# Performance work log

Hardware: AMD Instinct MI355X
Metric: run time of the kernel (lower is better)

The kernel has to match this reference:

```python
import math
import jax, jax.numpy as jnp
import numpy as np

B, S, D, H = 2, 2048, 1024, 16
HD = D // H  # head_dim = 64


def setup_inputs() -> dict:
    key = jax.random.key(0)
    k1, k2, k3 = jax.random.split(key, 3)
    scale = 0.02
    return {
        "x": jax.random.normal(k1, (B, S, D), dtype=jnp.float32),
        "w_qkv": jax.random.normal(k2, (D, 3 * D), dtype=jnp.float32) * scale,
        "b_qkv": jnp.zeros((3 * D,), dtype=jnp.float32),
        "w_proj": jax.random.normal(k3, (D, D), dtype=jnp.float32) * scale,
        "b_proj": jnp.zeros((D,), dtype=jnp.float32),
    }


def reference(x, w_qkv, b_qkv, w_proj, b_proj):
    bsz, seq_len, d_model = x.shape
    # fused qkv projection: [B,S,3D] -> [3,B,H,S,HD]
    qkv = (x @ w_qkv + b_qkv).reshape(bsz, seq_len, 3, H, HD)
    qkv = jnp.transpose(qkv, (2, 0, 3, 1, 4))
    q, k, v = qkv[0], qkv[1], qkv[2]
    # scores [B,H,S,S]
    scores = jnp.einsum("bhqd,bhkd->bhqk", q, k) / math.sqrt(HD)
    causal = jnp.tril(jnp.ones((seq_len, seq_len), dtype=bool))
    scores = jnp.where(causal[None, None], scores, -jnp.inf)
    probs = jax.nn.softmax(scores, axis=-1)
    # dropout = 0.0 (eval mode)
    context = jnp.einsum("bhqk,bhkd->bhqd", probs, v)
    context = jnp.transpose(context, (0, 2, 1, 3)).reshape(bsz, seq_len, d_model)
    return context @ w_proj + b_proj
```

## Files before the change

### kernel.cpp

```cpp
#include <hip/hip_runtime.h>

#define B_ 2
#define S_ 2048
#define D_ 1024
#define H_ 16
#define HD_ 64
#define M_ (B_*S_)
#define N_QKV (3*D_)

typedef __attribute__((ext_vector_type(8))) short short8;
typedef __attribute__((ext_vector_type(4))) float floatx4;

__device__ __forceinline__ float fast_exp2(float x) {
    return __builtin_amdgcn_exp2f(x);
}

__device__ __forceinline__ unsigned short f2b(float f) {
    union { float f; unsigned int u; } v; v.f = f;
    unsigned int u = v.u;
    u += 0x7FFFu + ((u >> 16) & 1u);
    return (unsigned short)(u >> 16);
}
__device__ __forceinline__ unsigned short f2b_fast(float f) {
    union { float f; unsigned int u; } v; v.f = f;
    return (unsigned short)((v.u + 0x8000u) >> 16);
}

__device__ __forceinline__ void glds16(const unsigned short* g, unsigned short* lds) {
    __builtin_amdgcn_global_load_lds(
        (const __attribute__((address_space(1))) unsigned int*)g,
        (__attribute__((address_space(3))) unsigned int*)lds, 16, 0, 0);
}

__global__ void cast_bf16_kernel(const float* __restrict__ src,
                                 unsigned short* __restrict__ dst, int n) {
    int i = (blockIdx.x * blockDim.x + threadIdx.x) * 4;
    if (i >= n) return;
    float4 f = *(const float4*)(src + i);
    ushort4 o;
    o.x = f2b(f.x); o.y = f2b(f.y); o.z = f2b(f.z); o.w = f2b(f.w);
    *(ushort4*)(dst + i) = o;
}

__global__ void transpose_cast_kernel(const float* __restrict__ W,
                                      unsigned short* __restrict__ Wt,
                                      int rows, int cols) {
    __shared__ float tile[32][33];
    int c0 = blockIdx.x * 32, r0 = blockIdx.y * 32;
    int tx = threadIdx.x, ty = threadIdx.y;
    #pragma unroll
    for (int i = 0; i < 4; ++i)
        tile[ty + i*8][tx] = W[(size_t)(r0 + ty + i*8) * cols + c0 + tx];
    __syncthreads();
    #pragma unroll
    for (int i = 0; i < 4; ++i)
        Wt[(size_t)(c0 + ty + i*8) * rows + r0 + tx] = f2b(tile[tx][ty + i*8]);
}

__global__ void vtrans_kernel(const unsigned short* __restrict__ V,
                              unsigned short* __restrict__ Vt) {
    __shared__ unsigned short L[64][72];
    const int t = threadIdx.x;
    const int s0 = blockIdx.x * 64;
    const int bh = blockIdx.y;
    {
        const int sl = t >> 2;
        const int hc = (t & 3) * 16;
        const unsigned short* src = V + ((size_t)bh * S_ + s0 + sl) * HD_ + hc;
        unsigned short tmp[16];
        *(uint4*)&tmp[0] = *(const uint4*)&src[0];
        *(uint4*)&tmp[8] = *(const uint4*)&src[8];
        #pragma unroll
        for (int j = 0; j < 16; ++j) {
            int r = hc + j;
            int pc = sl ^ (16 * ((r >> 4) & 3));
            L[r][pc] = tmp[j];
        }
    }
    __syncthreads();
    {
        const int hl = t >> 2;
        const int sc = (t & 3) * 16;
        const int g = 16 * ((hl >> 4) & 3);
        unsigned short* dst = Vt + ((size_t)bh * HD_ + hl) * S_ + s0 + sc;
        *(uint4*)&dst[0] = *(const uint4*)&L[hl][(sc ^ g) + 0];
        *(uint4*)&dst[8] = *(const uint4*)&L[hl][(sc ^ g) + 8];
    }
}

__global__ __launch_bounds__(256) void gemm_bt_kernel(
    const unsigned short* __restrict__ A,
    const unsigned short* __restrict__ Bt,
    const float* __restrict__ bias,
    unsigned short* __restrict__ q,
    unsigned short* __restrict__ k_,
    unsigned short* __restrict__ v,
    int Kdim)
{
    __shared__ unsigned short As[128*32];
    __shared__ unsigned short Bs[128*32];

    const int t = threadIdx.x;
    const int lane = t & 63;
    const int w = t >> 6;
    const int wm = w >> 1, wn = w & 1;
    const int quad = lane >> 4, l15 = lane & 15;
    const int bm = blockIdx.y, bn = blockIdx.x;

    const int srow = w*16 + (lane >> 2);
    const int scol = (lane & 3) * 8;

    const unsigned short* gA = A  + (size_t)(bm*128 + srow) * Kdim + scol;
    const unsigned short* gB = Bt + (size_t)(bn*128 + srow) * Kdim + scol;
    const size_t rowstep = (size_t)64 * Kdim;

    unsigned short* lA0 = As + (w*16)*32;
    unsigned short* lA1 = As + (64 + w*16)*32;
    unsigned short* lB0 = Bs + (w*16)*32;
    unsigned short* lB1 = Bs + (64 + w*16)*32;

    floatx4 acc[4][4];
    #pragma unroll
    for (int i = 0; i < 4; ++i)
        #pragma unroll
        for (int j = 0; j < 4; ++j)
            acc[i][j] = (floatx4){0.f, 0.f, 0.f, 0.f};

    for (int k0 = 0; k0 < Kdim; k0 += 32) {
        glds16(gA + k0,           lA0);
        glds16(gA + rowstep + k0, lA1);
        glds16(gB + k0,           lB0);
        glds16(gB + rowstep + k0, lB1);
        __syncthreads();
        short8 af[4], bfr[4];
        #pragma unroll
        for (int i = 0; i < 4; ++i)
            af[i] = *(const short8*)&As[(wm*64 + i*16 + l15)*32 + quad*8];
        #pragma unroll
        for (int j = 0; j < 4; ++j)
            bfr[j] = *(const short8*)&Bs[(wn*64 + j*16 + l15)*32 + quad*8];
        #pragma unroll
        for (int i = 0; i < 4; ++i)
            #pragma unroll
            for (int j = 0; j < 4; ++j)
                acc[i][j] = __builtin_amdgcn_mfma_f32_16x16x32_bf16(af[i], bfr[j], acc[i][j], 0, 0, 0);
        __syncthreads();
    }

    const float QSCALE = 0.18033688011112042f;

    #pragma unroll
    for (int i = 0; i < 4; ++i) {
        #pragma unroll
        for (int j = 0; j < 4; ++j) {
            #pragma unroll
            for (int reg = 0; reg < 4; ++reg) {
                int gm = bm*128 + wm*64 + i*16 + quad*4 + reg;
                int gn = bn*128 + wn*64 + j*16 + l15;
                float val = acc[i][j][reg] + bias[gn];
                int b = gm >> 11, s = gm & (S_ - 1);
                int which = gn >> 10, rem = gn & 1023;
                int h = rem >> 6, hd = rem & 63;
                if (which == 0) val *= QSCALE;
                unsigned short bv = f2b(val);
                size_t idx = ((size_t)(b*H_ + h) * S_ + s) * HD_ + hd;
                if (which == 0)      q[idx]  = bv;
                else if (which == 1) k_[idx] = bv;
                else                 v[idx]  = bv;
            }
        }
    }
}

__global__ __launch_bounds__(256) void gemm_bt64_kernel(
    const unsigned short* __restrict__ A,
    const unsigned short* __restrict__ Bt,
    const float* __restrict__ bias,
    float* __restrict__ outf,
    int Ndim, int Kdim)
{
    __shared__ unsigned short As[128*32];
    __shared__ unsigned short Bs[64*32];

    const int t = threadIdx.x;
    const int lane = t & 63;
    const int w = t >> 6;
    const int quad = lane >> 4, l15 = lane & 15;
    const int bm = blockIdx.y, bn = blockIdx.x;

    const int srow = w*16 + (lane >> 2);
    const int scol = (lane & 3) * 8;

    const unsigned short* gA = A  + (size_t)(bm*128 + srow) * Kdim + scol;
    const unsigned short* gB = Bt + (size_t)(bn*64  + srow) * Kdim + scol;
    const size_t rowstep = (size_t)64 * Kdim;

    unsigned short* lA0 = As + (w*16)*32;
    unsigned short* lA1 = As + (64 + w*16)*32;
    unsigned short* lB0 = Bs + (w*16)*32;

    floatx4 acc[2][4];
    #pragma unroll
    for (int i = 0; i < 2; ++i)
        #pragma unroll
        for (int j = 0; j < 4; ++j)
            acc[i][j] = (floatx4){0.f, 0.f, 0.f, 0.f};

    for (int k0 = 0; k0 < Kdim; k0 += 32) {
        glds16(gA + k0,           lA0);
        glds16(gA + rowstep + k0, lA1);
        glds16(gB + k0,           lB0);
        __syncthreads();
        short8 af[2], bfr[4];
        #pragma unroll
        for (int i = 0; i < 2; ++i)
            af[i] = *(const short8*)&As[(w*32 + i*16 + l15)*32 + quad*8];
        #pragma unroll
        for (int j = 0; j < 4; ++j)
            bfr[j] = *(const short8*)&Bs[(j*16 + l15)*32 + quad*8];
        #pragma unroll
        for (int i = 0; i < 2; ++i)
            #pragma unroll
            for (int j = 0; j < 4; ++j)
                acc[i][j] = __builtin_amdgcn_mfma_f32_16x16x32_bf16(af[i], bfr[j], acc[i][j], 0, 0, 0);
        __syncthreads();
    }

    #pragma unroll
    for (int i = 0; i < 2; ++i) {
        #pragma unroll
        for (int j = 0; j < 4; ++j) {
            #pragma unroll
            for (int reg = 0; reg < 4; ++reg) {
                int gm = bm*128 + w*32 + i*16 + quad*4 + reg;
                int gn = bn*64 + j*16 + l15;
                outf[(size_t)gm * Ndim + gn] = acc[i][j][reg] + bias[gn];
            }
        }
    }
}

__global__ __launch_bounds__(256, 2) void attn_kernel(
    const unsigned short* __restrict__ Q,
    const unsigned short* __restrict__ K,
    const unsigned short* __restrict__ Vt,
    unsigned short* __restrict__ ctx)
{
    __shared__ unsigned short KVs[2][2][64*64];
    __shared__ unsigned short Pt[4][2][16][72];

    const int t = threadIdx.x;
    const int lane = t & 63, w = t >> 6;
    const int quad = lane >> 4, l15 = lane & 15;
    const int bh = blockIdx.x & 31;
    const int a  = blockIdx.x >> 5;
    const int Hc = 31 - a;
    const int Lc = a;

    const unsigned short* Qh  = Q  + (size_t)bh * S_ * HD_;
    const unsigned short* Kh  = K  + (size_t)bh * S_ * HD_;
    const unsigned short* Vth = Vt + (size_t)bh * HD_ * S_;

    const int sr = t >> 3, sc = t & 7;
    const int gch = sc ^ (sr & 7);

    auto stage = [&](int j, int d) {
        unsigned short* kb = &KVs[d][0][0];
        unsigned short* vb = &KVs[d][1][0];
        const unsigned short* gk = Kh  + (size_t)(j*64 + sr)*HD_ + gch*8;
        const unsigned short* gv = Vth + (size_t)sr*S_ + (size_t)j*64 + gch*8;
        glds16(gk,                  kb + (w*8)*64);
        glds16(gk + 32*HD_,         kb + (32 + w*8)*64);
        glds16(gv,                  vb + (w*8)*64);
        glds16(gv + (size_t)32*S_,  vb + (32 + w*8)*64);
    };

    const int qH = Hc*64 + w*16;
    const int qL = Lc*64 + w*16;

    short8 bqH[2], bqL[2];
    #pragma unroll
    for (int kk = 0; kk < 2; ++kk) {
        bqH[kk] = *(const short8*)&Qh[(size_t)(qH + l15)*HD_ + kk*32 + quad*8];
        bqL[kk] = *(const short8*)&Qh[(size_t)(qL + l15)*HD_ + kk*32 + quad*8];
    }

    floatx4 OH[4], OL[4];
    #pragma unroll
    for (int nb = 0; nb < 4; ++nb) {
        OH[nb] = (floatx4){0.f,0.f,0.f,0.f};
        OL[nb] = (floatx4){0.f,0.f,0.f,0.f};
    }
    float lH = 0.f, lL = 0.f;

    auto do_tile = [&](const short8 (&bq)[2], floatx4 (&O)[4], float& l_acc,
                       int qbase, bool diag, int j, int ps,
                       const short8 (&ak)[4][2], const short8 (&av)[4][2]) {
        float z[4][4];
        #pragma unroll
        for (int nb = 0; nb < 4; ++nb) {
            floatx4 c = (floatx4){0.f,0.f,0.f,0.f};
            c = __builtin_amdgcn_mfma_f32_16x16x32_bf16(ak[nb][0], bq[0], c, 0,0,0);
            c = __builtin_amdgcn_mfma_f32_16x16x32_bf16(ak[nb][1], bq[1], c, 0,0,0);
            #pragma unroll
            for (int r = 0; r < 4; ++r) z[nb][r] = c[r];
        }
        if (diag) {
            const int qg = qbase + l15, koff = j*64;
            #pragma unroll
            for (int nb = 0; nb < 4; ++nb)
                #pragma unroll
                for (int r = 0; r < 4; ++r)
                    if (koff + nb*16 + quad*4 + r > qg) z[nb][r] = -1e30f;
        }
        float rs = 0.f;
        #pragma unroll
        for (int nb = 0; nb < 4; ++nb) {
            float p0 = fast_exp2(z[nb][0]);
            float p1 = fast_exp2(z[nb][1]);
            float p2 = fast_exp2(z[nb][2]);
            float p3 = fast_exp2(z[nb][3]);
            rs += (p0 + p1) + (p2 + p3);
            ushort4 pk;
            pk.x = f2b_fast(p0); pk.y = f2b_fast(p1);
            pk.z = f2b_fast(p2); pk.w = f2b_fast(p3);
            *(ushort4*)&Pt[w][ps][l15][nb*16 + quad*4] = pk;
        }
        l_acc += rs;
        short8 bp0 = *(const short8*)&Pt[w][ps][l15][quad*8];
        short8 bp1 = *(const short8*)&Pt[w][ps][l15][32 + quad*8];
        #pragma unroll
        for (int nb = 0; nb < 4; ++nb) {
            O[nb] = __builtin_amdgcn_mfma_f32_16x16x32_bf16(av[nb][0], bp0, O[nb], 0,0,0);
            O[nb] = __builtin_amdgcn_mfma_f32_16x16x32_bf16(av[nb][1], bp1, O[nb], 0,0,0);
        }
    };

    stage(0, 0);

    for (int j = 0; j <= Hc; ++j) {
        __syncthreads();
        if (j < Hc) stage(j+1, (j+1)&1);
        const int d = j & 1;
        const unsigned short* Ksb = &KVs[d][0][0];
        const unsigned short* Vsb = &KVs[d][1][0];

        short8 ak[4][2], av[4][2];
        #pragma unroll
        for (int nb = 0; nb < 4; ++nb)
            #pragma unroll
            for (int kk = 0; kk < 2; ++kk) {
                int off = (nb*16 + l15)*64 + (((quad + 4*kk) ^ (l15 & 7)) * 8);
                ak[nb][kk] = *(const short8*)&Ksb[off];
                av[nb][kk] = *(const short8*)&Vsb[off];
            }

        do_tile(bqH, OH, lH, qH, j == Hc, j, 0, ak, av);
        if (j <= Lc)
            do_tile(bqL, OL, lL, qL, j == Lc, j, 1, ak, av);
    }

    const int b = bh >> 4, h = bh & (H_ - 1);
    auto finish = [&](floatx4 (&O)[4], float l_acc, int qbase) {
        l_acc += __shfl_xor(l_acc, 16, 64);
        l_acc += __shfl_xor(l_acc, 32, 64);
        const float inv = 1.f / l_acc;
        const int qg = qbase + l15;
        #pragma unroll
        for (int nb = 0; nb < 4; ++nb) {
            ushort4 o;
            o.x = f2b(O[nb][0] * inv);
            o.y = f2b(O[nb][1] * inv);
            o.z = f2b(O[nb][2] * inv);
            o.w = f2b(O[nb][3] * inv);
            *(ushort4*)&ctx[((size_t)(b*S_ + qg))*D_ + h*HD_ + nb*16 + quad*4] = o;
        }
    };
    finish(OH, lH, qH);
    finish(OL, lL, qL);
}

extern "C" void kernel_launch(void* const* d_in, const int* in_sizes, int n_in,
                              void* d_out, int out_size, void* d_ws, size_t ws_size,
                              hipStream_t stream) {
    const float* x      = (const float*)d_in[0];
    const float* w_qkv  = (const float*)d_in[1];
    const float* b_qkv  = (const float*)d_in[2];
    const float* w_proj = (const float*)d_in[3];
    const float* b_proj = (const float*)d_in[4];
    float* out = (float*)d_out;

    unsigned short* xb     = (unsigned short*)d_ws;
    unsigned short* wqkvT  = xb     + (size_t)M_ * D_;
    unsigned short* wprojT = wqkvT  + (size_t)N_QKV * D_;
    unsigned short* Qb     = wprojT + (size_t)D_ * D_;
    unsigned short* Kb     = Qb     + (size_t)B_*H_*S_*HD_;
    unsigned short* Vb     = Kb     + (size_t)B_*H_*S_*HD_;
    unsigned short* Vtb    = Vb     + (size_t)B_*H_*S_*HD_;
    unsigned short* ctx    = xb;

    cast_bf16_kernel<<<dim3((M_*D_/4 + 255)/256), dim3(256), 0, stream>>>(x, xb, M_*D_);
    transpose_cast_kernel<<<dim3(N_QKV/32, D_/32), dim3(32, 8), 0, stream>>>(w_qkv, wqkvT, D_, N_QKV);
    transpose_cast_kernel<<<dim3(D_/32, D_/32), dim3(32, 8), 0, stream>>>(w_proj, wprojT, D_, D_);

    gemm_bt_kernel<<<dim3(N_QKV/128, M_/128), dim3(256), 0, stream>>>(
        xb, wqkvT, b_qkv, Qb, Kb, Vb, D_);

    vtrans_kernel<<<dim3(S_/64, B_*H_), dim3(256), 0, stream>>>(Vb, Vtb);

    attn_kernel<<<dim3(512), dim3(256), 0, stream>>>(Qb, Kb, Vtb, ctx);

    gemm_bt64_kernel<<<dim3(D_/64, M_/128), dim3(256), 0, stream>>>(
        ctx, wprojT, b_proj, out, D_, D_);
}
```

Before: 183.8 us.

## Fuse V transpose into QKV GEMM epilogue and widen GEMM K-tiles with swizzle

The QKV GEMM now writes V directly in transposed layout, which removes the separate vtrans kernel launch and its extra round trip through global memory. Both GEMMs move to a 64-wide K tile with XOR-swizzled LDS staging to cut bank conflicts and halve the number of barriers. Operands are swapped so the epilogue issues vectorized stores for Q, K and the output. Occupancy hints are added, and the attention kernel raises wave priority around its MFMA blocks. The transposed V stores are scalar and strided, which may cost more than the kernel they replace.

Result: faster. 174.2 us (-5.2%).

```diff
diff --git a/kernel.cpp b/kernel.cpp
--- a/kernel.cpp
+++ b/kernel.cpp
@@ -57,48 +57,17 @@
         Wt[(size_t)(c0 + ty + i*8) * rows + r0 + tx] = f2b(tile[tx][ty + i*8]);
 }
 
-__global__ void vtrans_kernel(const unsigned short* __restrict__ V,
-                              unsigned short* __restrict__ Vt) {
-    __shared__ unsigned short L[64][72];
-    const int t = threadIdx.x;
-    const int s0 = blockIdx.x * 64;
-    const int bh = blockIdx.y;
-    {
-        const int sl = t >> 2;
-        const int hc = (t & 3) * 16;
-        const unsigned short* src = V + ((size_t)bh * S_ + s0 + sl) * HD_ + hc;
-        unsigned short tmp[16];
-        *(uint4*)&tmp[0] = *(const uint4*)&src[0];
-        *(uint4*)&tmp[8] = *(const uint4*)&src[8];
-        #pragma unroll
-        for (int j = 0; j < 16; ++j) {
-            int r = hc + j;
-            int pc = sl ^ (16 * ((r >> 4) & 3));
-            L[r][pc] = tmp[j];
-        }
-    }
-    __syncthreads();
-    {
-        const int hl = t >> 2;
-        const int sc = (t & 3) * 16;
-        const int g = 16 * ((hl >> 4) & 3);
-        unsigned short* dst = Vt + ((size_t)bh * HD_ + hl) * S_ + s0 + sc;
-        *(uint4*)&dst[0] = *(const uint4*)&L[hl][(sc ^ g) + 0];
-        *(uint4*)&dst[8] = *(const uint4*)&L[hl][(sc ^ g) + 8];
-    }
-}
-
-__global__ __launch_bounds__(256) void gemm_bt_kernel(
+__global__ __launch_bounds__(256, 3) void gemm_bt_kernel(
     const unsigned short* __restrict__ A,
     const unsigned short* __restrict__ Bt,
     const float* __restrict__ bias,
     unsigned short* __restrict__ q,
     unsigned short* __restrict__ k_,
-    unsigned short* __restrict__ v,
+    unsigned short* __restrict__ vt,
     int Kdim)
 {
-    __shared__ unsigned short As[128*32];
-    __shared__ unsigned short Bs[128*32];
+    __shared__ unsigned short As[128*64];
+    __shared__ unsigned short Bs[128*64];
 
     const int t = threadIdx.x;
     const int lane = t & 63;
@@ -107,17 +76,17 @@
     const int quad = lane >> 4, l15 = lane & 15;
     const int bm = blockIdx.y, bn = blockIdx.x;
 
-    const int srow = w*16 + (lane >> 2);
-    const int scol = (lane & 3) * 8;
-
-    const unsigned short* gA = A  + (size_t)(bm*128 + srow) * Kdim + scol;
-    const unsigned short* gB = Bt + (size_t)(bn*128 + srow) * Kdim + scol;
-    const size_t rowstep = (size_t)64 * Kdim;
-
-    unsigned short* lA0 = As + (w*16)*32;
-    unsigned short* lA1 = As + (64 + w*16)*32;
-    unsigned short* lB0 = Bs + (w*16)*32;
-    unsigned short* lB1 = Bs + (64 + w*16)*32;
+    const int sr32 = t >> 3;
+    const int gch  = (t & 7) ^ (sr32 & 7);
+
+    const unsigned short* gA = A  + (size_t)(bm*128 + sr32) * Kdim + gch*8;
+    const unsigned short* gB = Bt + (size_t)(bn*128 + sr32) * Kdim + gch*8;
+    const size_t rstep = (size_t)32 * Kdim;
+
+    unsigned short* lA = As + (w*8)*64;
+    unsigned short* lB = Bs + (w*8)*64;
+
+    const int swz = (l15 & 7);
 
     floatx4 acc[4][4];
     #pragma unroll
@@ -126,61 +95,76 @@
         for (int j = 0; j < 4; ++j)
             acc[i][j] = (floatx4){0.f, 0.f, 0.f, 0.f};
 
-    for (int k0 = 0; k0 < Kdim; k0 += 32) {
-        glds16(gA + k0,           lA0);
-        glds16(gA + rowstep + k0, lA1);
-        glds16(gB + k0,           lB0);
-        glds16(gB + rowstep + k0, lB1);
+    for (int k0 = 0; k0 < Kdim; k0 += 64) {
+        #pragma unroll
+        for (int c = 0; c < 4; ++c) {
+            glds16(gA + c*rstep + k0, lA + c*2048);
+            glds16(gB + c*rstep + k0, lB + c*2048);
+        }
         __syncthreads();
-        short8 af[4], bfr[4];
+        short8 an[4][2], am[4][2];
         #pragma unroll
         for (int i = 0; i < 4; ++i)
-            af[i] = *(const short8*)&As[(wm*64 + i*16 + l15)*32 + quad*8];
-        #pragma unroll
-        for (int j = 0; j < 4; ++j)
-            bfr[j] = *(const short8*)&Bs[(wn*64 + j*16 + l15)*32 + quad*8];
-        #pragma unroll
-        for (int i = 0; i < 4; ++i)
-            #pragma unroll
-            for (int j = 0; j < 4; ++j)
-                acc[i][j] = __builtin_amdgcn_mfma_f32_16x16x32_bf16(af[i], bfr[j], acc[i][j], 0, 0, 0);
+            #pragma unroll
+            for (int kk = 0; kk < 2; ++kk) {
+                const int coff = ((quad + 4*kk) ^ swz) * 8;
+                an[i][kk] = *(const short8*)&Bs[(wn*64 + i*16 + l15)*64 + coff];
+                am[i][kk] = *(const short8*)&As[(wm*64 + i*16 + l15)*64 + coff];
+            }
+        #pragma unroll
+        for (int kk = 0; kk < 2; ++kk)
+            #pragma unroll
+            for (int i = 0; i < 4; ++i)
+                #pragma unroll
+                for (int j = 0; j < 4; ++j)
+                    acc[i][j] = __builtin_amdgcn_mfma_f32_16x16x32_bf16(an[i][kk], am[j][kk], acc[i][j], 0, 0, 0);
         __syncthreads();
     }
 
     const float QSCALE = 0.18033688011112042f;
+    const int which = bn >> 3;
+    const int hcol  = (bn & 7)*2 + wn;
+    const int b     = bm >> 4;
+    const int sbase = (bm & 15)*128 + wm*64;
 
     #pragma unroll
     for (int i = 0; i < 4; ++i) {
+        float4 bias4 = *(const float4*)&bias[bn*128 + wn*64 + i*16 + quad*4];
+        const int hd0 = i*16 + quad*4;
         #pragma unroll
         for (int j = 0; j < 4; ++j) {
-            #pragma unroll
-            for (int reg = 0; reg < 4; ++reg) {
-                int gm = bm*128 + wm*64 + i*16 + quad*4 + reg;
-                int gn = bn*128 + wn*64 + j*16 + l15;
-                float val = acc[i][j][reg] + bias[gn];
-                int b = gm >> 11, s = gm & (S_ - 1);
-                int which = gn >> 10, rem = gn & 1023;
-                int h = rem >> 6, hd = rem & 63;
-                if (which == 0) val *= QSCALE;
-                unsigned short bv = f2b(val);
-                size_t idx = ((size_t)(b*H_ + h) * S_ + s) * HD_ + hd;
-                if (which == 0)      q[idx]  = bv;
-                else if (which == 1) k_[idx] = bv;
-                else                 v[idx]  = bv;
+            const int srow = sbase + j*16 + l15;
+            float v0 = acc[i][j][0] + bias4.x;
+            float v1 = acc[i][j][1] + bias4.y;
+            float v2 = acc[i][j][2] + bias4.z;
+            float v3 = acc[i][j][3] + bias4.w;
+            if (which == 0) {
+                v0 *= QSCALE; v1 *= QSCALE; v2 *= QSCALE; v3 *= QSCALE;
+                ushort4 o; o.x = f2b(v0); o.y = f2b(v1); o.z = f2b(v2); o.w = f2b(v3);
+                *(ushort4*)&q[((size_t)(b*H_ + hcol) * S_ + srow) * HD_ + hd0] = o;
+            } else if (which == 1) {
+                ushort4 o; o.x = f2b(v0); o.y = f2b(v1); o.z = f2b(v2); o.w = f2b(v3);
+                *(ushort4*)&k_[((size_t)(b*H_ + hcol) * S_ + srow) * HD_ + hd0] = o;
+            } else {
+                const size_t vb = (size_t)(b*H_ + hcol) * HD_ + hd0;
+                vt[(vb + 0) * S_ + srow] = f2b(v0);
+                vt[(vb + 1) * S_ + srow] = f2b(v1);
+                vt[(vb + 2) * S_ + srow] = f2b(v2);
+                vt[(vb + 3) * S_ + srow] = f2b(v3);
             }
         }
     }
 }
 
-__global__ __launch_bounds__(256) void gemm_bt64_kernel(
+__global__ __launch_bounds__(256, 2) void gemm_bt64_kernel(
     const unsigned short* __restrict__ A,
     const unsigned short* __restrict__ Bt,
     const float* __restrict__ bias,
     float* __restrict__ outf,
     int Ndim, int Kdim)
 {
-    __shared__ unsigned short As[128*32];
-    __shared__ unsigned short Bs[64*32];
+    __shared__ unsigned short As[128*64];
+    __shared__ unsigned short Bs[64*64];
 
     const int t = threadIdx.x;
     const int lane = t & 63;
@@ -188,54 +172,66 @@
     const int quad = lane >> 4, l15 = lane & 15;
     const int bm = blockIdx.y, bn = blockIdx.x;
 
-    const int srow = w*16 + (lane >> 2);
-    const int scol = (lane & 3) * 8;
-
-    const unsigned short* gA = A  + (size_t)(bm*128 + srow) * Kdim + scol;
-    const unsigned short* gB = Bt + (size_t)(bn*64  + srow) * Kdim + scol;
-    const size_t rowstep = (size_t)64 * Kdim;
-
-    unsigned short* lA0 = As + (w*16)*32;
-    unsigned short* lA1 = As + (64 + w*16)*32;
-    unsigned short* lB0 = Bs + (w*16)*32;
-
-    floatx4 acc[2][4];
-    #pragma unroll
-    for (int i = 0; i < 2; ++i)
-        #pragma unroll
-        for (int j = 0; j < 4; ++j)
+    const int sr32 = t >> 3;
+    const int gch  = (t & 7) ^ (sr32 & 7);
+
+    const unsigned short* gA = A  + (size_t)(bm*128 + sr32) * Kdim + gch*8;
+    const unsigned short* gB = Bt + (size_t)(bn*64  + sr32) * Kdim + gch*8;
+    const size_t rstep = (size_t)32 * Kdim;
+
+    unsigned short* lA = As + (w*8)*64;
+    unsigned short* lB = Bs + (w*8)*64;
+
+    const int swz = (l15 & 7);
+
+    floatx4 acc[4][2];
+    #pragma unroll
+    for (int i = 0; i < 4; ++i)
+        #pragma unroll
+        for (int j = 0; j < 2; ++j)
             acc[i][j] = (floatx4){0.f, 0.f, 0.f, 0.f};
 
-    for (int k0 = 0; k0 < Kdim; k0 += 32) {
-        glds16(gA + k0,           lA0);
-        glds16(gA + rowstep + k0, lA1);
-        glds16(gB + k0,           lB0);
+    for (int k0 = 0; k0 < Kdim; k0 += 64) {
+        #pragma unroll
+        for (int c = 0; c < 4; ++c)
+            glds16(gA + c*rstep + k0, lA + c*2048);
+        #pragma unroll
+        for (int c = 0; c < 2; ++c)
+            glds16(gB + c*rstep + k0, lB + c*2048);
         __syncthreads();
-        short8 af[2], bfr[4];
-        #pragma unroll
-        for (int i = 0; i < 2; ++i)
-            af[i] = *(const short8*)&As[(w*32 + i*16 + l15)*32 + quad*8];
-        #pragma unroll
-        for (int j = 0; j < 4; ++j)
-            bfr[j] = *(const short8*)&Bs[(j*16 + l15)*32 + quad*8];
-        #pragma unroll
-        for (int i = 0; i < 2; ++i)
-            #pragma unroll
-            for (int j = 0; j < 4; ++j)
-                acc[i][j] = __builtin_amdgcn_mfma_f32_16x16x32_bf16(af[i], bfr[j], acc[i][j], 0, 0, 0);
+        short8 an[4][2], am[2][2];
+        #pragma unroll
+        for (int kk = 0; kk < 2; ++kk) {
+            const int coff = ((quad + 4*kk) ^ swz) * 8;
+            #pragma unroll
+            for (int i = 0; i < 4; ++i)
+                an[i][kk] = *(const short8*)&Bs[(i*16 + l15)*64 + coff];
+            #pragma unroll
+            for (int j = 0; j < 2; ++j)
+                am[j][kk] = *(const short8*)&As[(w*32 + j*16 + l15)*64 + coff];
+        }
+        #pragma unroll
+        for (int kk = 0; kk < 2; ++kk)
+            #pragma unroll
+            for (int i = 0; i < 4; ++i)
+                #pragma unroll
+                for (int j = 0; j < 2; ++j)
+                    acc[i][j] = __builtin_amdgcn_mfma_f32_16x16x32_bf16(an[i][kk], am[j][kk], acc[i][j], 0, 0, 0);
         __syncthreads();
     }
 
     #pragma unroll
-    for (int i = 0; i < 2; ++i) {
-        #pragma unroll
-        for (int j = 0; j < 4; ++j) {
-            #pragma unroll
-            for (int reg = 0; reg < 4; ++reg) {
-                int gm = bm*128 + w*32 + i*16 + quad*4 + reg;
-                int gn = bn*64 + j*16 + l15;
-                outf[(size_t)gm * Ndim + gn] = acc[i][j][reg] + bias[gn];
-            }
+    for (int i = 0; i < 4; ++i) {
+        float4 bias4 = *(const float4*)&bias[bn*64 + i*16 + quad*4];
+        #pragma unroll
+        for (int j = 0; j < 2; ++j) {
+            const int gm = bm*128 + w*32 + j*16 + l15;
+            float4 o;
+            o.x = acc[i][j][0] + bias4.x;
+            o.y = acc[i][j][1] + bias4.y;
+            o.z = acc[i][j][2] + bias4.z;
+            o.w = acc[i][j][3] + bias4.w;
+            *(float4*)&outf[(size_t)gm * Ndim + bn*64 + i*16 + quad*4] = o;
         }
     }
 }
@@ -297,6 +293,7 @@
                        int qbase, bool diag, int j, int ps,
                        const short8 (&ak)[4][2], const short8 (&av)[4][2]) {
         float z[4][4];
+        __builtin_amdgcn_s_setprio(1);
         #pragma unroll
         for (int nb = 0; nb < 4; ++nb) {
             floatx4 c = (floatx4){0.f,0.f,0.f,0.f};
@@ -305,6 +302,7 @@
             #pragma unroll
             for (int r = 0; r < 4; ++r) z[nb][r] = c[r];
         }
+        __builtin_amdgcn_s_setprio(0);
         if (diag) {
             const int qg = qbase + l15, koff = j*64;
             #pragma unroll
@@ -329,11 +327,13 @@
         l_acc += rs;
         short8 bp0 = *(const short8*)&Pt[w][ps][l15][quad*8];
         short8 bp1 = *(const short8*)&Pt[w][ps][l15][32 + quad*8];
+        __builtin_amdgcn_s_setprio(1);
         #pragma unroll
         for (int nb = 0; nb < 4; ++nb) {
             O[nb] = __builtin_amdgcn_mfma_f32_16x16x32_bf16(av[nb][0], bp0, O[nb], 0,0,0);
             O[nb] = __builtin_amdgcn_mfma_f32_16x16x32_bf16(av[nb][1], bp1, O[nb], 0,0,0);
         }
+        __builtin_amdgcn_s_setprio(0);
     };
 
     stage(0, 0);
@@ -404,9 +404,7 @@
     transpose_cast_kernel<<<dim3(D_/32, D_/32), dim3(32, 8), 0, stream>>>(w_proj, wprojT, D_, D_);
 
     gemm_bt_kernel<<<dim3(N_QKV/128, M_/128), dim3(256), 0, stream>>>(
-        xb, wqkvT, b_qkv, Qb, Kb, Vb, D_);
-
-    vtrans_kernel<<<dim3(S_/64, B_*H_), dim3(256), 0, stream>>>(Vb, Vtb);
+        xb, wqkvT, b_qkv, Qb, Kb, Vtb, D_);
 
     attn_kernel<<<dim3(512), dim3(256), 0, stream>>>(Qb, Kb, Vtb, ctx);
 
```
